# Performance work log

Measured on AMD Instinct MI355X. Metric: run time of the kernel, lower is better.

## Reference

```python
import jax, jax.numpy as jnp
import numpy as np

EMBED_DIM = 1024
NUM_HEADS = 16
HEAD_DIM = EMBED_DIM // NUM_HEADS
WINDOW = 256


def setup_inputs() -> dict:
    key = jax.random.key(0)
    ks = jax.random.split(key, 9)
    B, S, E = 4, 4096, EMBED_DIM
    sc = 1.0 / np.sqrt(E)
    return {
        "x": jax.random.normal(ks[0], (B, S, E), jnp.float32),
        "Wq": jax.random.normal(ks[1], (E, E), jnp.float32) * sc,
        "bq": jax.random.normal(ks[2], (E,), jnp.float32) * 0.01,
        "Wk": jax.random.normal(ks[3], (E, E), jnp.float32) * sc,
        "bk": jax.random.normal(ks[4], (E,), jnp.float32) * 0.01,
        "Wv": jax.random.normal(ks[5], (E, E), jnp.float32) * sc,
        "bv": jax.random.normal(ks[6], (E,), jnp.float32) * 0.01,
        "Wo": jax.random.normal(ks[7], (E, E), jnp.float32) * sc,
        "bo": jax.random.normal(ks[8], (E,), jnp.float32) * 0.01,
    }


def reference(x, Wq, bq, Wk, bk, Wv, bv, Wo, bo):
    B, S, E = x.shape
    H, D, W = NUM_HEADS, HEAD_DIM, WINDOW
    NW = S // W  # seq_len chosen divisible by window -> no padding

    def split_heads(t):  # [B,S,E] -> [B,H,NW,W,D]
        return t.reshape(B, S, H, D).transpose(0, 2, 1, 3).reshape(B, H, NW, W, D)

    q = split_heads(x @ Wq + bq)
    k = split_heads(x @ Wk + bk)
    v = split_heads(x @ Wv + bv)

    # block-diagonal attention within each non-overlapping window
    scores = jnp.einsum("bhnqd,bhnkd->bhnqk", q, k) / jnp.sqrt(
        jnp.asarray(D, x.dtype))
    attn = jax.nn.softmax(scores, axis=-1)
    out = jnp.einsum("bhnqk,bhnkd->bhnqd", attn, v)  # [B,H,NW,W,D]

    out = out.reshape(B, H, S, D).transpose(0, 2, 1, 3).reshape(B, S, E)
    return out @ Wo + bo
```

## Files before the change

### kernel.cpp

```cpp
#include <hip/hip_runtime.h>

typedef __bf16 bf16x8 __attribute__((ext_vector_type(8)));
typedef float  f32x4  __attribute__((ext_vector_type(4)));

#define MFMA(a,b,c) __builtin_amdgcn_mfma_f32_16x16x32_bf16((a),(b),(c),0,0,0)
#define SB() __builtin_amdgcn_sched_barrier(0)

__device__ __forceinline__ unsigned short f2bf(float f){
  unsigned u = __builtin_bit_cast(unsigned, f);
  u += 0x7fffu + ((u>>16)&1u);
  return (unsigned short)(u>>16);
}
__device__ __forceinline__ unsigned pack_bf2(float a, float b){
  return (unsigned)f2bf(a) | ((unsigned)f2bf(b)<<16);
}
__device__ __forceinline__ void gload_lds16(const void* g, void* l){
  __builtin_amdgcn_global_load_lds((__attribute__((address_space(1))) void*)(g),
                                   (__attribute__((address_space(3))) void*)(l), 16, 0, 0);
}

__global__ void k_cvt_x(const float* __restrict__ x, unsigned short* __restrict__ o){
  const size_t t = (size_t)blockIdx.x*256 + threadIdx.x;
  #pragma unroll
  for (int i=0;i<4;i++){
    size_t idx = t + (size_t)i*1048576;
    float4 f = ((const float4*)x)[idx];
    ((uint2*)o)[idx] = make_uint2(pack_bf2(f.x,f.y), pack_bf2(f.z,f.w));
  }
}

__global__ void k_cvt_wT(const float* __restrict__ Wq, const float* __restrict__ Wk,
                         const float* __restrict__ Wv, const float* __restrict__ Wo,
                         unsigned short* __restrict__ wT){
  const int z = blockIdx.z;
  const float* W = (z==0)?Wq:(z==1)?Wk:(z==2)?Wv:Wo;
  unsigned short* out = wT + (size_t)z*1048576;
  __shared__ float tile[32][33];
  const int r0 = blockIdx.y*32, c0 = blockIdx.x*32;
  const int r = threadIdx.x>>5, c = threadIdx.x&31;
  #pragma unroll
  for (int i=0;i<4;i++) tile[r + i*8][c] = W[(size_t)(r0 + r + i*8)*1024 + c0 + c];
  __syncthreads();
  #pragma unroll
  for (int i=0;i<4;i++)
    out[(size_t)(c0 + r + i*8)*1024 + r0 + c] = f2bf(tile[c][r + i*8]);
}

#define QUAD16(AF, BF, MF0) do { \
  _Pragma("unroll") \
  for (int mf_=0; mf_<4; ++mf_){ \
    _Pragma("unroll") \
    for (int nf_=0; nf_<4; ++nf_) \
      acc[MF0+mf_][nf_] = MFMA(AF[mf_], BF[nf_], acc[MF0+mf_][nf_]); \
  } } while(0)

template<int MODE>
__global__ __launch_bounds__(512,2) void k_gemm8(const unsigned short* __restrict__ A,
                       const unsigned short* __restrict__ Bm,
                       const float* __restrict__ bias0, const float* __restrict__ bias1,
                       const float* __restrict__ bias2,
                       unsigned short* __restrict__ q_ws, unsigned short* __restrict__ k_ws,
                       unsigned short* __restrict__ v_ws, float* __restrict__ outf)
{
  __shared__ char smem[131072];
  const int tid = threadIdx.x, lane = tid&63, wid = tid>>6;
  const int g = lane>>4, l15 = lane&15;
  const int wr = wid>>2, wc = wid&3;

  constexpr int NBX = (MODE==0)? 12 : 4;
  constexpr int CPX = (MODE==0)? 96 : 32;
  const int flat = blockIdx.y*NBX + blockIdx.x;
  const int swz  = (flat&7)*CPX + (flat>>3);
  const int m0 = (swz/NBX)<<8, n0 = (swz%NBX)<<8;

  auto stageH = [&](int isA, int tt, int hf){
    char* ldst = smem + (isA?0:65536) + (tt&1)*32768 + hf*16384 + wid*1024;
    const unsigned short* gbase = isA? A : Bm;
    const int row0 = (isA? m0 : n0) + hf*128;
    #pragma unroll
    for (int j=0;j<2;j++){
      const int o = (j*512 + tid)*16;
      const int r = o>>7, cb = o&127;
      const int cs = cb ^ ((r&7)<<4);
      gload_lds16((const char*)gbase + (size_t)(row0 + r)*2048 + (tt<<7) + cs,
                  ldst + j*8192);
    }
  };

  f32x4 acc[8][4];
  #pragma unroll
  for (int i=0;i<8;i++)
    #pragma unroll
    for (int j=0;j<4;j++) acc[i][j] = f32x4{0.f,0.f,0.f,0.f};

  stageH(1,0,0); stageH(1,0,1);
  stageH(0,0,0); stageH(0,0,1);
  stageH(1,1,0); stageH(1,1,1);
  asm volatile("s_waitcnt vmcnt(4)" ::: "memory");
  __builtin_amdgcn_s_barrier();
  SB();

  const int sw = (l15&7)<<4;
  for (int t=0;t<16;++t){
    const char* Ab = smem + (t&1)*32768 + wr*16384;
    const char* Bb = smem + 65536 + (t&1)*32768 + (wc>>1)*16384;
    const int brow = (wc&1)*64;
    bf16x8 aK0[4], aK1[4], bK0[4], bK1[4];

    #pragma unroll
    for (int mf=0;mf<4;mf++)
      aK0[mf] = *(const bf16x8*)(Ab + (mf*16+l15)*128 + ((g*16) ^ sw));
    #pragma unroll
    for (int nf=0;nf<4;nf++)
      bK0[nf] = *(const bf16x8*)(Bb + (brow+nf*16+l15)*128 + ((g*16) ^ sw));
    if (t+1 < 16) stageH(0, t+1, 0);
    SB();
    __builtin_amdgcn_s_barrier();
    asm volatile("s_waitcnt lgkmcnt(0)" ::: "memory");
    SB();
    __builtin_amdgcn_s_setprio(1);
    QUAD16(aK0, bK0, 0);
    __builtin_amdgcn_s_setprio(0);
    SB();
    __builtin_amdgcn_s_barrier();
    SB();

    #pragma unroll
    for (int mf=0;mf<4;mf++)
      aK1[mf] = *(const bf16x8*)(Ab + (mf*16+l15)*128 + ((64+g*16) ^ sw));
    #pragma unroll
    for (int nf=0;nf<4;nf++)
      bK1[nf] = *(const bf16x8*)(Bb + (brow+nf*16+l15)*128 + ((64+g*16) ^ sw));
    if (t+1 < 16) stageH(0, t+1, 1);
    SB();
    __builtin_amdgcn_s_barrier();
    asm volatile("s_waitcnt lgkmcnt(0)" ::: "memory");
    SB();
    __builtin_amdgcn_s_setprio(1);
    QUAD16(aK1, bK1, 0);
    __builtin_amdgcn_s_setprio(0);
    SB();
    __builtin_amdgcn_s_barrier();
    SB();

    #pragma unroll
    for (int mf=0;mf<4;mf++)
      aK0[mf] = *(const bf16x8*)(Ab + ((4+mf)*16+l15)*128 + ((g*16) ^ sw));
    #pragma unroll
    for (int mf=0;mf<4;mf++)
      aK1[mf] = *(const bf16x8*)(Ab + ((4+mf)*16+l15)*128 + ((64+g*16) ^ sw));
    SB();
    __builtin_amdgcn_s_barrier();
    asm volatile("s_waitcnt lgkmcnt(0)" ::: "memory");
    SB();
    __builtin_amdgcn_s_setprio(1);
    QUAD16(aK0, bK0, 4);
    __builtin_amdgcn_s_setprio(0);
    SB();
    __builtin_amdgcn_s_barrier();
    SB();

    if (t+2 < 16){ stageH(1, t+2, 0); stageH(1, t+2, 1); }
    SB();
    __builtin_amdgcn_s_barrier();
    SB();
    __builtin_amdgcn_s_setprio(1);
    QUAD16(aK1, bK1, 4);
    __builtin_amdgcn_s_setprio(0);
    SB();
    if (t < 14)       asm volatile("s_waitcnt vmcnt(4)" ::: "memory");
    else if (t == 14) asm volatile("s_waitcnt vmcnt(0)" ::: "memory");
    __builtin_amdgcn_s_barrier();
    SB();
  }

  if constexpr (MODE==0){
    const int z  = n0>>10;
    const int nE = n0 & 1023;
    const float* bias = (z==0)? bias0 : (z==1)? bias1 : bias2;
    #pragma unroll
    for (int nf=0;nf<4;nf++){
      const int ncol = nE + wc*64 + nf*16 + l15;
      const float bn = bias[ncol];
      const int h = ncol>>6, d = ncol&63;
      #pragma unroll
      for (int mf=0;mf<8;mf++){
        const int mb = m0 + wr*128 + mf*16 + g*4;
        if (z==2){
          const int b = mb>>12, s = mb&4095, nw = s>>8, w0 = s&255;
          unsigned short pk0=f2bf(acc[mf][nf][0]+bn), pk1=f2bf(acc[mf][nf][1]+bn),
                         pk2=f2bf(acc[mf][nf][2]+bn), pk3=f2bf(acc[mf][nf][3]+bn);
          size_t idx = ((((size_t)(b*16+h)*16 + nw)*64 + d)<<8) + w0;
          *(ushort4*)(v_ws + idx) = make_ushort4(pk0,pk1,pk2,pk3);
        } else {
          unsigned short* dst = (z==0)? q_ws : k_ws;
          const float scale = (z==0)? 0.125f : 1.0f;
          #pragma unroll
          for (int r=0;r<4;r++){
            const int m = mb + r, b = m>>12, s = m&4095;
            dst[(((size_t)(b*16+h)*4096 + s)<<6) + d] = f2bf((acc[mf][nf][r]+bn)*scale);
          }
        }
      }
    }
  } else {
    #pragma unroll
    for (int nf=0;nf<4;nf++){
      const int n = n0 + wc*64 + nf*16 + l15;
      const float bn = bias0[n];
      #pragma unroll
      for (int mf=0;mf<8;mf++)
        #pragma unroll
        for (int r=0;r<4;r++){
          const int m = m0 + wr*128 + mf*16 + g*4 + r;
          outf[(size_t)m*1024 + n] = acc[mf][nf][r] + bn;
        }
    }
  }
}

__global__ __launch_bounds__(256,2) void k_attn(const unsigned short* __restrict__ qw,
                                                const unsigned short* __restrict__ kw,
                                                const unsigned short* __restrict__ vw,
                                                unsigned short* __restrict__ ow)
{
  __shared__ unsigned short Ks[2][4096];
  __shared__ unsigned short Vs[2][4096];
  __shared__ unsigned short Ps[4][4096];
  const int tid = threadIdx.x, lane = tid&63, wid = tid>>6;
  const int g = lane>>4, l15 = lane&15;
  const int bhn = blockIdx.x;
  const int nw = bhn&15, h = (bhn>>4)&15, b = bhn>>8;

  const size_t qkbase = ((size_t)((b*16+h)*4096 + nw*256))<<6;
  const unsigned short* Qg = qw + qkbase;
  const unsigned short* Kg = kw + qkbase;
  const unsigned short* Vg = vw + (((size_t)(b*16+h)*16 + nw)<<14);
  const float NEG_INF = -__builtin_inff();

  bf16x8 qa[4][2];
  #pragma unroll
  for (int qf=0;qf<4;qf++)
    #pragma unroll
    for (int ks=0;ks<2;ks++)
      qa[qf][ks] = *(const bf16x8*)((const char*)Qg + (wid*64 + qf*16 + l15)*128 + ks*64 + g*16);

  auto stage = [&](int kt, int bi){
    #pragma unroll
    for (int i=0;i<4;i++){
      const int chunk = wid*4 + i;
      const int obase = (chunk&7)<<10;
      const int o = obase + lane*16;
      const int r = o>>7, cb = o&127;
      const int cs = cb ^ ((r&7)<<4);
      if (chunk < 8)
        gload_lds16((const char*)Kg + (kt*64 + r)*128 + cs, (char*)Ks[bi] + obase);
      else
        gload_lds16((const char*)Vg + r*512 + kt*128 + cs, (char*)Vs[bi] + obase);
    }
  };

  f32x4 oacc[4][4];
  float mrow[4][4], lrow[4][4];
  #pragma unroll
  for (int i=0;i<4;i++)
    #pragma unroll
    for (int j=0;j<4;j++){ oacc[i][j] = f32x4{0.f,0.f,0.f,0.f}; mrow[i][j] = NEG_INF; lrow[i][j] = 0.f; }

  stage(0,0);
  __syncthreads();
  for (int kt=0;kt<4;kt++){
    const int cur = kt&1;
    if (kt<3) stage(kt+1, cur^1);

    bf16x8 kb[4][2];
    #pragma unroll
    for (int kf=0;kf<4;kf++)
      #pragma unroll
      for (int ks=0;ks<2;ks++){
        const int kr = kf*16 + l15, cb = ks*64 + g*16;
        kb[kf][ks] = *(const bf16x8*)((const char*)Ks[cur] + kr*128 + (cb ^ ((kr&7)<<4)));
      }

    unsigned short* P = Ps[wid];
    #pragma unroll
    for (int qf=0;qf<4;qf++){
      f32x4 sfr[4];
      #pragma unroll
      for (int kf=0;kf<4;kf++){
        f32x4 zz = f32x4{0.f,0.f,0.f,0.f};
        zz = MFMA(qa[qf][0], kb[kf][0], zz);
        sfr[kf] = MFMA(qa[qf][1], kb[kf][1], zz);
      }
      #pragma unroll
      for (int r=0;r<4;r++){
        float t = fmaxf(fmaxf(sfr[0][r],sfr[1][r]), fmaxf(sfr[2][r],sfr[3][r]));
        t = fmaxf(t, __shfl_xor(t,1,64)); t = fmaxf(t, __shfl_xor(t,2,64));
        t = fmaxf(t, __shfl_xor(t,4,64)); t = fmaxf(t, __shfl_xor(t,8,64));
        const float mo = mrow[qf][r];
        const float mn = fmaxf(mo, t);
        const float alpha = __expf(mo - mn);
        float rs = 0.f;
        #pragma unroll
        for (int kf=0;kf<4;kf++){ float p = __expf(sfr[kf][r]-mn); sfr[kf][r] = p; rs += p; }
        rs += __shfl_xor(rs,1,64); rs += __shfl_xor(rs,2,64);
        rs += __shfl_xor(rs,4,64); rs += __shfl_xor(rs,8,64);
        lrow[qf][r] = lrow[qf][r]*alpha + rs;
        mrow[qf][r] = mn;
        #pragma unroll
        for (int df=0;df<4;df++) oacc[qf][df][r] *= alpha;
        const int prow = qf*16 + g*4 + r;
        const int sw = (prow&7)<<4;
        char* Pb = (char*)P + prow*128;
        #pragma unroll
        for (int kf=0;kf<4;kf++)
          *(unsigned short*)(Pb + (((kf*16 + l15)*2) ^ sw)) = f2bf(sfr[kf][r]);
      }
    }
    __builtin_amdgcn_sched_barrier(0);

    bf16x8 vb[4][2];
    #pragma unroll
    for (int df=0;df<4;df++)
      #pragma unroll
      for (int ks=0;ks<2;ks++){
        const int d = df*16 + l15, cb = ks*64 + g*16;
        vb[df][ks] = *(const bf16x8*)((const char*)Vs[cur] + d*128 + (cb ^ ((d&7)<<4)));
      }
    #pragma unroll
    for (int qf=0;qf<4;qf++){
      const int pr = qf*16 + l15;
      const bf16x8 pa0 = *(const bf16x8*)((const char*)P + pr*128 + ((g*16)      ^ ((pr&7)<<4)));
      const bf16x8 pa1 = *(const bf16x8*)((const char*)P + pr*128 + ((64 + g*16) ^ ((pr&7)<<4)));
      #pragma unroll
      for (int df=0;df<4;df++){
        oacc[qf][df] = MFMA(pa0, vb[df][0], oacc[qf][df]);
        oacc[qf][df] = MFMA(pa1, vb[df][1], oacc[qf][df]);
      }
    }
    __syncthreads();
  }

  #pragma unroll
  for (int qf=0;qf<4;qf++)
    #pragma unroll
    for (int r=0;r<4;r++){
      const float inv = 1.f / lrow[qf][r];
      const int srow = nw*256 + wid*64 + qf*16 + g*4 + r;
      const size_t base = ((size_t)b*4096 + srow)*1024 + (size_t)h*64;
      #pragma unroll
      for (int df=0;df<4;df++)
        ow[base + df*16 + l15] = f2bf(oacc[qf][df][r]*inv);
    }
}

extern "C" void kernel_launch(void* const* d_in, const int* in_sizes, int n_in,
                              void* d_out, int out_size, void* d_ws, size_t ws_size,
                              hipStream_t stream)
{
  const float* x  = (const float*)d_in[0];
  const float* Wq = (const float*)d_in[1];
  const float* bq = (const float*)d_in[2];
  const float* Wk = (const float*)d_in[3];
  const float* bk = (const float*)d_in[4];
  const float* Wv = (const float*)d_in[5];
  const float* bv = (const float*)d_in[6];
  const float* Wo = (const float*)d_in[7];
  const float* bo = (const float*)d_in[8];
  float* out = (float*)d_out;

  char* ws = (char*)d_ws;
  unsigned short* xbf  = (unsigned short*)(ws);
  unsigned short* wT   = (unsigned short*)(ws + (size_t)32*1048576);
  unsigned short* q_ws = (unsigned short*)(ws + (size_t)40*1048576);
  unsigned short* k_ws = (unsigned short*)(ws + (size_t)72*1048576);
  unsigned short* v_ws = (unsigned short*)(ws + (size_t)104*1048576);
  unsigned short* obf  = xbf;

  k_cvt_x<<<4096,256,0,stream>>>(x, xbf);
  k_cvt_wT<<<dim3(32,32,4),256,0,stream>>>(Wq,Wk,Wv,Wo, wT);
  k_gemm8<0><<<dim3(12,64),512,0,stream>>>(xbf, wT, bq,bk,bv, q_ws,k_ws,v_ws, nullptr);
  k_attn<<<1024,256,0,stream>>>(q_ws,k_ws,v_ws, obf);
  k_gemm8<1><<<dim3(4,64),512,0,stream>>>(obf, wT + (size_t)3*1048576, bo,nullptr,nullptr,
                                          nullptr,nullptr,nullptr, out);
}
```

Measured before the change: 260.0 us.

## Software-pipeline LDS fragment reads one MFMA quadrant ahead in GEMM main loop

Restructures the GEMM K-loop so the LDS reads for the next MFMA quadrant are issued before the current quadrant's MFMAs, using ping-pong register fragments. The first fragments of the next tile are prefetched at the end of each iteration. This removes the old read, barrier, wait, compute serialization and cuts barriers per quadrant. It adds register pressure at 512 threads with 2 blocks per SM, and it depends on the reordered vmcnt waits and barriers staying correct.

```diff
diff --git a/kernel.cpp b/kernel.cpp
--- a/kernel.cpp
+++ b/kernel.cpp
@@ -5,6 +5,7 @@
 
 #define MFMA(a,b,c) __builtin_amdgcn_mfma_f32_16x16x32_bf16((a),(b),(c),0,0,0)
 #define SB() __builtin_amdgcn_sched_barrier(0)
+#define LGKM0 asm volatile("s_waitcnt lgkmcnt(0)" ::: "memory")
 
 __device__ __forceinline__ unsigned short f2bf(float f){
   unsigned u = __builtin_bit_cast(unsigned, f);
@@ -53,6 +54,18 @@
     for (int nf_=0; nf_<4; ++nf_) \
       acc[MF0+mf_][nf_] = MFMA(AF[mf_], BF[nf_], acc[MF0+mf_][nf_]); \
   } } while(0)
+
+#define READ_A(DST, MF0, KOFF, AB) do { \
+  _Pragma("unroll") \
+  for (int mf_=0; mf_<4; ++mf_) \
+    DST[mf_] = *(const bf16x8*)((AB) + (((MF0)+mf_)*16+l15)*128 + (((KOFF)+g*16) ^ sw)); \
+  } while(0)
+
+#define READ_B(DST, KOFF, BB) do { \
+  _Pragma("unroll") \
+  for (int nf_=0; nf_<4; ++nf_) \
+    DST[nf_] = *(const bf16x8*)((BB) + (brow+nf_*16+l15)*128 + (((KOFF)+g*16) ^ sw)); \
+  } while(0)
 
 template<int MODE>
 __global__ __launch_bounds__(512,2) void k_gemm8(const unsigned short* __restrict__ A,
@@ -93,84 +106,76 @@
     #pragma unroll
     for (int j=0;j<4;j++) acc[i][j] = f32x4{0.f,0.f,0.f,0.f};
 
+  const int sw = (l15&7)<<4;
+  const int brow = (wc&1)*64;
+  bf16x8 A0f[4], A1f[4], B0f[4], B1f[4];
+
   stageH(1,0,0); stageH(1,0,1);
   stageH(0,0,0); stageH(0,0,1);
   stageH(1,1,0); stageH(1,1,1);
   asm volatile("s_waitcnt vmcnt(4)" ::: "memory");
   __builtin_amdgcn_s_barrier();
   SB();
-
-  const int sw = (l15&7)<<4;
+  {
+    const char* Ab0 = smem + wr*16384;
+    const char* Bb0 = smem + 65536 + (wc>>1)*16384;
+    READ_A(A0f, 0, 0, Ab0);
+    READ_B(B0f, 0, Bb0);
+  }
+
+  #pragma unroll 1
   for (int t=0;t<16;++t){
-    const char* Ab = smem + (t&1)*32768 + wr*16384;
-    const char* Bb = smem + 65536 + (t&1)*32768 + (wc>>1)*16384;
-    const int brow = (wc&1)*64;
-    bf16x8 aK0[4], aK1[4], bK0[4], bK1[4];
-
-    #pragma unroll
-    for (int mf=0;mf<4;mf++)
-      aK0[mf] = *(const bf16x8*)(Ab + (mf*16+l15)*128 + ((g*16) ^ sw));
-    #pragma unroll
-    for (int nf=0;nf<4;nf++)
-      bK0[nf] = *(const bf16x8*)(Bb + (brow+nf*16+l15)*128 + ((g*16) ^ sw));
+    const char* Abc = smem + (t&1)*32768 + wr*16384;
+    const char* Bbc = smem + 65536 + (t&1)*32768 + (wc>>1)*16384;
+    const char* Abn = smem + ((t+1)&1)*32768 + wr*16384;
+    const char* Bbn = smem + 65536 + ((t+1)&1)*32768 + (wc>>1)*16384;
+
+    LGKM0; SB();
+    __builtin_amdgcn_s_barrier(); SB();
+    READ_A(A1f, 4, 0, Abc);
     if (t+1 < 16) stageH(0, t+1, 0);
     SB();
-    __builtin_amdgcn_s_barrier();
-    asm volatile("s_waitcnt lgkmcnt(0)" ::: "memory");
-    SB();
     __builtin_amdgcn_s_setprio(1);
-    QUAD16(aK0, bK0, 0);
+    QUAD16(A0f, B0f, 0);
     __builtin_amdgcn_s_setprio(0);
     SB();
-    __builtin_amdgcn_s_barrier();
-    SB();
-
-    #pragma unroll
-    for (int mf=0;mf<4;mf++)
-      aK1[mf] = *(const bf16x8*)(Ab + (mf*16+l15)*128 + ((64+g*16) ^ sw));
-    #pragma unroll
-    for (int nf=0;nf<4;nf++)
-      bK1[nf] = *(const bf16x8*)(Bb + (brow+nf*16+l15)*128 + ((64+g*16) ^ sw));
+
+    LGKM0; SB();
+    __builtin_amdgcn_s_barrier(); SB();
+    READ_A(A0f, 0, 64, Abc);
+    READ_B(B1f, 64, Bbc);
     if (t+1 < 16) stageH(0, t+1, 1);
     SB();
-    __builtin_amdgcn_s_barrier();
-    asm volatile("s_waitcnt lgkmcnt(0)" ::: "memory");
-    SB();
     __builtin_amdgcn_s_setprio(1);
-    QUAD16(aK1, bK1, 0);
+    QUAD16(A1f, B0f, 4);
     __builtin_amdgcn_s_setprio(0);
     SB();
-    __builtin_amdgcn_s_barrier();
-    SB();
-
-    #pragma unroll
-    for (int mf=0;mf<4;mf++)
-      aK0[mf] = *(const bf16x8*)(Ab + ((4+mf)*16+l15)*128 + ((g*16) ^ sw));
-    #pragma unroll
-    for (int mf=0;mf<4;mf++)
-      aK1[mf] = *(const bf16x8*)(Ab + ((4+mf)*16+l15)*128 + ((64+g*16) ^ sw));
-    SB();
-    __builtin_amdgcn_s_barrier();
-    asm volatile("s_waitcnt lgkmcnt(0)" ::: "memory");
+
+    LGKM0; SB();
+    __builtin_amdgcn_s_barrier(); SB();
+    READ_A(A1f, 4, 64, Abc);
     SB();
     __builtin_amdgcn_s_setprio(1);
-    QUAD16(aK0, bK0, 4);
+    QUAD16(A0f, B1f, 0);
     __builtin_amdgcn_s_setprio(0);
     SB();
-    __builtin_amdgcn_s_barrier();
-    SB();
-
+
+    LGKM0; SB();
+    __builtin_amdgcn_s_barrier(); SB();
     if (t+2 < 16){ stageH(1, t+2, 0); stageH(1, t+2, 1); }
-    SB();
-    __builtin_amdgcn_s_barrier();
+    if (t+1 < 16){
+      if (t+2 < 16) asm volatile("s_waitcnt vmcnt(4)" ::: "memory");
+      else          asm volatile("s_waitcnt vmcnt(0)" ::: "memory");
+    }
+    __builtin_amdgcn_s_barrier(); SB();
+    if (t+1 < 16){
+      READ_A(A0f, 0, 0, Abn);
+      READ_B(B0f, 0, Bbn);
+    }
     SB();
     __builtin_amdgcn_s_setprio(1);
-    QUAD16(aK1, bK1, 4);
+    QUAD16(A1f, B1f, 4);
     __builtin_amdgcn_s_setprio(0);
-    SB();
-    if (t < 14)       asm volatile("s_waitcnt vmcnt(4)" ::: "memory");
-    else if (t == 14) asm volatile("s_waitcnt vmcnt(0)" ::: "memory");
-    __builtin_amdgcn_s_barrier();
     SB();
   }
 
```

Result: no change. 263.0 us (+1.2%).
